# Optimization experiments

Measured on AMD Instinct MI355X. Metric: run time of the kernel, lower is better.

The kernel has to match this reference:

```python
import jax, jax.numpy as jnp
import numpy as np

SIZE = 1024
LATENT_DIM = 256
BETA_C = 0.25
LEGACY = True


def setup_inputs() -> dict:
    key = jax.random.key(0)
    k1, k2 = jax.random.split(key)
    z = jax.random.normal(k1, (8, LATENT_DIM, 16, 16, 16), dtype=jnp.float32)
    # nn.Embedding weight initialized uniform(-1/size, 1/size)
    embedding = jax.random.uniform(
        k2, (SIZE, LATENT_DIM), minval=-1.0 / SIZE, maxval=1.0 / SIZE, dtype=jnp.float32
    )
    return {"z": z, "embedding": embedding}


def reference(z, embedding):
    sg = jax.lax.stop_gradient
    B, C, D, H, W = z.shape
    # [B, D, H, W, C]
    zp = jnp.transpose(z, (0, 2, 3, 4, 1))
    zf = zp.reshape(-1, C)  # [N, C]
    # pairwise squared distances [N, K]
    d = (
        jnp.sum(zf * zf, axis=1, keepdims=True)
        + jnp.sum(embedding * embedding, axis=1)
        - 2.0 * (zf @ embedding.T)
    )
    idx = jnp.argmin(d, axis=1)  # [N]
    # direct gather == one-hot @ embedding
    z_q = embedding[idx].reshape(zp.shape)
    if LEGACY:
        loss = jnp.mean((sg(z_q) - zp) ** 2) + BETA_C * jnp.mean((z_q - sg(zp)) ** 2)
    else:
        loss = BETA_C * jnp.mean((sg(z_q) - zp) ** 2) + jnp.mean((z_q - sg(zp)) ** 2)
    # perplexity: e_mean = mean of one-hot encodings == normalized counts
    counts = jnp.zeros((SIZE,), dtype=z.dtype).at[idx].add(1.0)
    e_mean = counts / zf.shape[0]
    perplexity = jnp.exp(-jnp.sum(e_mean * jnp.log(e_mean + 1e-10)))
    # straight-through estimator
    z_q = zp + sg(z_q - zp)
    z_q = jnp.transpose(z_q, (0, 4, 1, 2, 3))  # back to [B, C, D, H, W]
    return z_q, loss, perplexity, idx
```

## Files before the change

kernel.cpp:

```cpp
#include <hip/hip_runtime.h>
#include <cstddef>
#include <cstdint>

#define CDIM 256
#define SPAT 4096
#define KCODE 1024

#define LOSS_OFF 8388608
#define PERP_OFF 8388609
#define IDX_OFF  8388610

typedef __bf16 bf16x8 __attribute__((ext_vector_type(8)));
typedef float floatx16 __attribute__((ext_vector_type(16)));
typedef unsigned short ushort8 __attribute__((ext_vector_type(8)));

__device__ __forceinline__ unsigned short f2bf_rne(float f) {
    union { float f; uint32_t u; } c; c.f = f;
    uint32_t u = c.u;
    return (unsigned short)((u + 0x7fffu + ((u >> 16) & 1u)) >> 16);
}
__device__ __forceinline__ float bf2f(unsigned short h) {
    union { float f; uint32_t u; } c; c.u = ((uint32_t)h) << 16;
    return c.f;
}

__device__ __forceinline__ void dma16(const void* g, void* l) {
    __builtin_amdgcn_global_load_lds(
        (const __attribute__((address_space(1))) void*)g,
        (__attribute__((address_space(3))) void*)l, 16, 0, 0);
}

__global__ __launch_bounds__(256) void vq_prep(const float* __restrict__ emb,
                                               unsigned short* __restrict__ ehsw,
                                               unsigned short* __restrict__ elsw,
                                               float* __restrict__ enorm,
                                               float* __restrict__ counts,
                                               float* __restrict__ losssum,
                                               unsigned long long* __restrict__ pbm) {
    int tid = threadIdx.x;
    if (blockIdx.x == 0) {
        for (int i = tid; i < KCODE; i += 256) counts[i] = 0.0f;
        if (tid == 0) losssum[0] = 0.0f;
    }
    if (tid < 128) pbm[blockIdx.x * 128 + tid] = 0xFFFFFFFFFFFFFFFFull;

    int w = tid >> 6, lane = tid & 63;
    int k = blockIdx.x * 4 + w;
    const float* row = emb + (size_t)k * CDIM;
    float s = 0.0f;
#pragma unroll
    for (int i = 0; i < 4; ++i) {
        float v = row[lane + 64 * i];
        s = fmaf(v, v, s);
    }
#pragma unroll
    for (int m = 32; m > 0; m >>= 1) s += __shfl_xor(s, m, 64);
    if (lane == 0) enorm[k] = s;

    float4 v4 = *(const float4*)(row + lane * 4);
    unsigned short h0 = f2bf_rne(v4.x), h1 = f2bf_rne(v4.y),
                   h2 = f2bf_rne(v4.z), h3 = f2bf_rne(v4.w);
    ushort4 hv = make_ushort4(h0, h1, h2, h3);
    ushort4 lv = make_ushort4(f2bf_rne(v4.x - bf2f(h0)), f2bf_rne(v4.y - bf2f(h1)),
                              f2bf_rne(v4.z - bf2f(h2)), f2bf_rne(v4.w - bf2f(h3)));
    int kb = lane >> 1, cj = (lane & 1) * 4;
    int st = k >> 5, ks = k & 31;
    int phys = kb ^ (ks & 7);
    size_t dst = (size_t)st * 8192 + ks * 256 + phys * 8 + cj;
    *(ushort4*)(ehsw + dst) = hv;
    *(ushort4*)(elsw + dst) = lv;
}

__global__ __launch_bounds__(256, 2) void vq_dist(const float* __restrict__ z,
                                                  const unsigned short* __restrict__ ehsw,
                                                  const unsigned short* __restrict__ elsw,
                                                  const float* __restrict__ enorm,
                                                  unsigned long long* __restrict__ pbm) {
    __shared__ __align__(16) unsigned char lds[65536 + 2048 + 512];
    float* zhalf = (float*)lds;
    float* ens_s = (float*)(lds + 65536);
    float* zzs   = (float*)(lds + 67584);

    const int tid = threadIdx.x;
    const int w = tid >> 6;
    const int lane = tid & 63;
    const int m_ = lane & 31;
    const int g = lane >> 5;
    const int bid = blockIdx.x;
    const int pos = bid >> 1;
    const int kh = bid & 1;
    const int ch = w & 1;
    const int hlf = w >> 1;
    const int n0 = pos * 128;
    const int b = n0 >> 12;
    const int sp0 = n0 & 4095;
    const float* zb = z + (size_t)b * CDIM * SPAT + sp0;
    const int stg0 = (bid >> 4) & 15;

    ushort8 zh[16], zl[16];

    for (int h = 0; h < 2; ++h) {
        for (int i = tid; i < CDIM * 16; i += 256) {
            int c = i >> 4, seg = i & 15;
            *(float4*)&zhalf[c * 64 + seg * 4] =
                *(const float4*)(zb + (size_t)c * SPAT + h * 64 + seg * 4);
        }
        __syncthreads();
        if (hlf == h) {
#pragma unroll
            for (int kc = 0; kc < 16; ++kc) {
#pragma unroll
                for (int j = 0; j < 8; ++j) {
                    float v = zhalf[(kc * 16 + g * 8 + j) * 64 + ch * 32 + m_];
                    unsigned short hb = f2bf_rne(v);
                    unsigned short lb = f2bf_rne(v - bf2f(hb));
                    zh[kc][j] = hb; zl[kc][j] = lb;
                }
            }
        } else if (w == (h == 0 ? 2 : 0)) {
            float s = 0.0f;
            for (int c = 0; c < CDIM; ++c) {
                float v = zhalf[c * 64 + lane];
                s = fmaf(v, v, s);
            }
            zzs[h * 64 + lane] = s;
        } else if (h == 0 && w == 3) {
            for (int i = lane; i < 512; i += 64) ens_s[i] = enorm[kh * 512 + i];
        }
        __syncthreads();
    }

    const float zzv = zzs[w * 32 + m_];

    float bs = 3.4e38f;
    int bi_ = 0;

    const int bufid = w >> 1;
    const int hf = w & 1;
    const char* gsrc = (const char*)(bufid ? elsw : ehsw);
    const int gs0 = kh * 16;

    {
        const char* gp = gsrc + ((size_t)(gs0 + stg0) << 14) + (hf << 13) + (lane << 4);
        char* lp = (char*)lds + ((size_t)bufid << 14) + (hf << 13);
#pragma unroll
        for (int j = 0; j < 8; ++j) dma16(gp + j * 1024, lp + j * 1024);
    }

    for (int s = 0; s < 16; ++s) {
        __syncthreads();
        if (s < 15) {
            const int se_n = (s + 1 + stg0) & 15;
            const char* gp = gsrc + ((size_t)(gs0 + se_n) << 14) + (hf << 13) + (lane << 4);
            char* lp = (char*)lds + (((size_t)(s + 1) & 1) << 15) +
                       ((size_t)bufid << 14) + (hf << 13);
#pragma unroll
            for (int j = 0; j < 8; ++j) dma16(gp + j * 1024, lp + j * 1024);
            __builtin_amdgcn_sched_barrier(0);
        }
        const char* EHb = (const char*)lds + (((size_t)s & 1) << 15);
        const char* ELb = EHb + 16384;

        floatx16 a = {0.0f, 0.0f, 0.0f, 0.0f, 0.0f, 0.0f, 0.0f, 0.0f,
                      0.0f, 0.0f, 0.0f, 0.0f, 0.0f, 0.0f, 0.0f, 0.0f};
#pragma unroll
        for (int kc = 0; kc < 16; ++kc) {
            int kb0 = kc * 2 + g;
            int off = m_ * 512 + ((kb0 ^ (m_ & 7)) << 4);
            bf16x8 aeh = *(const bf16x8*)(EHb + off);
            bf16x8 ael = *(const bf16x8*)(ELb + off);
            bf16x8 bh = __builtin_bit_cast(bf16x8, zh[kc]);
            bf16x8 bl = __builtin_bit_cast(bf16x8, zl[kc]);
            a = __builtin_amdgcn_mfma_f32_32x32x16_bf16(aeh, bh, a, 0, 0, 0);
            a = __builtin_amdgcn_mfma_f32_32x32x16_bf16(ael, bh, a, 0, 0, 0);
            a = __builtin_amdgcn_mfma_f32_32x32x16_bf16(aeh, bl, a, 0, 0, 0);
        }

        const int se = (s + stg0) & 15;
#pragma unroll
        for (int reg = 0; reg < 16; ++reg) {
            int mm = (reg & 3) + 8 * (reg >> 2) + 4 * g;
            int il = se * 32 + mm;
            float en = ens_s[il];
            float d = (zzv + en) - 2.0f * a[reg];
            int code = kh * 512 + il;
            if (d < bs || (d == bs && code < bi_)) { bs = d; bi_ = code; }
        }
    }

    {
        float s2 = __shfl_xor(bs, 32, 64);
        int i2 = __shfl_xor(bi_, 32, 64);
        if (s2 < bs || (s2 == bs && i2 < bi_)) { bs = s2; bi_ = i2; }
    }
    if (lane < 32) {
        unsigned long long key =
            ((unsigned long long)__float_as_uint(bs) << 32) | (unsigned int)bi_;
        atomicMin(&pbm[n0 + w * 32 + m_], key);
    }
}

__global__ __launch_bounds__(256) void vq_gather(const float* __restrict__ z,
                                                 const float* __restrict__ emb,
                                                 const unsigned long long* __restrict__ pbm,
                                                 float* __restrict__ counts,
                                                 float* __restrict__ losssum,
                                                 float* __restrict__ out) {
    __shared__ __align__(16) unsigned char lds[128 * 1040 + 512];
    int* bidxs = (int*)(lds + 133120);

    const int tid = threadIdx.x;
    const int w = tid >> 6;
    const int lane = tid & 63;
    const int n0 = blockIdx.x * 128;
    const int b = n0 >> 12;
    const int sp0 = n0 & 4095;
    const float* zb = z + (size_t)b * CDIM * SPAT + sp0;

    if (tid < 128) {
        int ki = (int)(unsigned int)(pbm[n0 + tid] & 0xFFFFFFFFull);
        bidxs[tid] = ki;
        out[IDX_OFF + n0 + tid] = (float)ki;
        atomicAdd(&counts[ki], 1.0f);
    }
    __syncthreads();

#pragma unroll
    for (int r = 0; r < 32; ++r) {
        int row = w * 32 + r;
        int k = bidxs[row];
        int slot = (row & 3) * 32 + (row >> 2);
        dma16((const char*)emb + ((size_t)k << 10) + (lane << 4),
              (char*)lds + (size_t)slot * 1040);
    }
    __syncthreads();

    float ls = 0.0f;
    float* outz = out + (size_t)b * CDIM * SPAT + sp0;
    const int col4 = tid & 31;
    const int c_0 = tid >> 5;
    const float* e0 = (const float*)((const char*)lds + (size_t)(0 * 32 + col4) * 1040);
    const float* e1 = (const float*)((const char*)lds + (size_t)(1 * 32 + col4) * 1040);
    const float* e2 = (const float*)((const char*)lds + (size_t)(2 * 32 + col4) * 1040);
    const float* e3 = (const float*)((const char*)lds + (size_t)(3 * 32 + col4) * 1040);
    for (int c = c_0; c < CDIM; c += 8) {
        float4 zp = *(const float4*)(zb + (size_t)c * SPAT + col4 * 4);
        float d0 = e0[c] - zp.x, d1 = e1[c] - zp.y,
              d2 = e2[c] - zp.z, d3 = e3[c] - zp.w;
        float4 o;
        o.x = zp.x + d0; o.y = zp.y + d1; o.z = zp.z + d2; o.w = zp.w + d3;
        ls = fmaf(d0, d0, ls); ls = fmaf(d1, d1, ls);
        ls = fmaf(d2, d2, ls); ls = fmaf(d3, d3, ls);
        *(float4*)(outz + (size_t)c * SPAT + col4 * 4) = o;
    }
#pragma unroll
    for (int m = 32; m > 0; m >>= 1) ls += __shfl_xor(ls, m, 64);
    if (lane == 0) atomicAdd(losssum, ls);
}

__global__ __launch_bounds__(256) void vq_finalize(const float* __restrict__ counts,
                                                   const float* __restrict__ losssum,
                                                   float* __restrict__ out) {
    __shared__ float red[256];
    int tid = threadIdx.x;
    float s = 0.0f;
    for (int k = tid; k < KCODE; k += 256) {
        float em = counts[k] * (1.0f / 32768.0f);
        s += em * logf(em + 1e-10f);
    }
    red[tid] = s;
    __syncthreads();
    for (int off = 128; off > 0; off >>= 1) {
        if (tid < off) red[tid] += red[tid + off];
        __syncthreads();
    }
    if (tid == 0) {
        float m = losssum[0] * (1.0f / 8388608.0f);
        out[LOSS_OFF] = m + 0.25f * m;
        out[PERP_OFF] = expf(-red[0]);
    }
}

extern "C" void kernel_launch(void* const* d_in, const int* in_sizes, int n_in,
                              void* d_out, int out_size, void* d_ws, size_t ws_size,
                              hipStream_t stream) {
    const float* z = (const float*)d_in[0];
    const float* emb = (const float*)d_in[1];
    float* out = (float*)d_out;
    unsigned long long* pbm = (unsigned long long*)d_ws;
    unsigned short* ehsw = (unsigned short*)(pbm + 32768);
    unsigned short* elsw = ehsw + (size_t)KCODE * CDIM;
    float* enorm = (float*)(elsw + (size_t)KCODE * CDIM);
    float* counts = enorm + KCODE;
    float* losssum = counts + KCODE;

    vq_prep<<<256, 256, 0, stream>>>(emb, ehsw, elsw, enorm, counts, losssum, pbm);
    vq_dist<<<512, 256, 0, stream>>>(z, ehsw, elsw, enorm, pbm);
    vq_gather<<<256, 256, 0, stream>>>(z, emb, pbm, counts, losssum, out);
    vq_finalize<<<1, 256, 0, stream>>>(counts, losssum, out);
}
```

Before: 179.8 us.

## Fuse gather epilogue into distance kernel via last-block-arrives flag

```diff
diff --git a/kernel.cpp b/kernel.cpp
--- a/kernel.cpp
+++ b/kernel.cpp
@@ -36,12 +36,14 @@
                                                float* __restrict__ enorm,
                                                float* __restrict__ counts,
                                                float* __restrict__ losssum,
-                                               unsigned long long* __restrict__ pbm) {
+                                               unsigned long long* __restrict__ pbm,
+                                               unsigned int* __restrict__ flags) {
     int tid = threadIdx.x;
     if (blockIdx.x == 0) {
         for (int i = tid; i < KCODE; i += 256) counts[i] = 0.0f;
         if (tid == 0) losssum[0] = 0.0f;
     }
+    if (blockIdx.x == 1) flags[tid] = 0u;
     if (tid < 128) pbm[blockIdx.x * 128 + tid] = 0xFFFFFFFFFFFFFFFFull;
 
     int w = tid >> 6, lane = tid & 63;
@@ -72,14 +74,20 @@
 }
 
 __global__ __launch_bounds__(256, 2) void vq_dist(const float* __restrict__ z,
+                                                  const float* __restrict__ emb,
                                                   const unsigned short* __restrict__ ehsw,
                                                   const unsigned short* __restrict__ elsw,
                                                   const float* __restrict__ enorm,
-                                                  unsigned long long* __restrict__ pbm) {
+                                                  unsigned long long* __restrict__ pbm,
+                                                  unsigned int* __restrict__ flags,
+                                                  float* __restrict__ counts,
+                                                  float* __restrict__ losssum,
+                                                  float* __restrict__ out) {
     __shared__ __align__(16) unsigned char lds[65536 + 2048 + 512];
     float* zhalf = (float*)lds;
     float* ens_s = (float*)(lds + 65536);
     float* zzs   = (float*)(lds + 67584);
+    __shared__ int last_s;
 
     const int tid = threadIdx.x;
     const int w = tid >> 6;
@@ -198,60 +206,56 @@
             ((unsigned long long)__float_as_uint(bs) << 32) | (unsigned int)bi_;
         atomicMin(&pbm[n0 + w * 32 + m_], key);
     }
-}
-
-__global__ __launch_bounds__(256) void vq_gather(const float* __restrict__ z,
-                                                 const float* __restrict__ emb,
-                                                 const unsigned long long* __restrict__ pbm,
-                                                 float* __restrict__ counts,
-                                                 float* __restrict__ losssum,
-                                                 float* __restrict__ out) {
-    __shared__ __align__(16) unsigned char lds[128 * 1040 + 512];
-    int* bidxs = (int*)(lds + 133120);
-
-    const int tid = threadIdx.x;
-    const int w = tid >> 6;
-    const int lane = tid & 63;
-    const int n0 = blockIdx.x * 128;
-    const int b = n0 >> 12;
-    const int sp0 = n0 & 4095;
-    const float* zb = z + (size_t)b * CDIM * SPAT + sp0;
-
+    __threadfence();
+    __syncthreads();
+    if (tid == 0) last_s = (atomicAdd(&flags[pos], 1u) == 1u);
+    __syncthreads();
+    if (!last_s) return;
+    __threadfence();
+
+    int* bidxs = (int*)(lds + 67584);
     if (tid < 128) {
-        int ki = (int)(unsigned int)(pbm[n0 + tid] & 0xFFFFFFFFull);
+        unsigned long long key = __hip_atomic_load(
+            &pbm[n0 + tid], __ATOMIC_RELAXED, __HIP_MEMORY_SCOPE_AGENT);
+        int ki = (int)(unsigned int)(key & 0xFFFFFFFFull);
         bidxs[tid] = ki;
         out[IDX_OFF + n0 + tid] = (float)ki;
         atomicAdd(&counts[ki], 1.0f);
     }
     __syncthreads();
 
-#pragma unroll
-    for (int r = 0; r < 32; ++r) {
-        int row = w * 32 + r;
-        int k = bidxs[row];
-        int slot = (row & 3) * 32 + (row >> 2);
-        dma16((const char*)emb + ((size_t)k << 10) + (lane << 4),
-              (char*)lds + (size_t)slot * 1040);
-    }
-    __syncthreads();
-
     float ls = 0.0f;
     float* outz = out + (size_t)b * CDIM * SPAT + sp0;
     const int col4 = tid & 31;
-    const int c_0 = tid >> 5;
-    const float* e0 = (const float*)((const char*)lds + (size_t)(0 * 32 + col4) * 1040);
-    const float* e1 = (const float*)((const char*)lds + (size_t)(1 * 32 + col4) * 1040);
-    const float* e2 = (const float*)((const char*)lds + (size_t)(2 * 32 + col4) * 1040);
-    const float* e3 = (const float*)((const char*)lds + (size_t)(3 * 32 + col4) * 1040);
-    for (int c = c_0; c < CDIM; c += 8) {
-        float4 zp = *(const float4*)(zb + (size_t)c * SPAT + col4 * 4);
-        float d0 = e0[c] - zp.x, d1 = e1[c] - zp.y,
-              d2 = e2[c] - zp.z, d3 = e3[c] - zp.w;
-        float4 o;
-        o.x = zp.x + d0; o.y = zp.y + d1; o.z = zp.z + d2; o.w = zp.w + d3;
-        ls = fmaf(d0, d0, ls); ls = fmaf(d1, d1, ls);
-        ls = fmaf(d2, d2, ls); ls = fmaf(d3, d3, ls);
-        *(float4*)(outz + (size_t)c * SPAT + col4 * 4) = o;
+    const int c_0t = tid >> 5;
+    const int col4h = col4 & 15;
+    for (int round = 0; round < 2; ++round) {
+#pragma unroll
+        for (int r = 0; r < 16; ++r) {
+            int row_local = w * 16 + r;
+            int k = bidxs[round * 64 + row_local];
+            int slot = (row_local & 3) * 16 + (row_local >> 2);
+            dma16((const char*)emb + ((size_t)k << 10) + (lane << 4),
+                  (char*)lds + (size_t)slot * 1040);
+        }
+        __syncthreads();
+        if ((col4 >> 4) == round) {
+            const float* e0 = (const float*)((const char*)lds + (size_t)(0 * 16 + col4h) * 1040);
+            const float* e1 = (const float*)((const char*)lds + (size_t)(1 * 16 + col4h) * 1040);
+            const float* e2 = (const float*)((const char*)lds + (size_t)(2 * 16 + col4h) * 1040);
+            const float* e3 = (const float*)((const char*)lds + (size_t)(3 * 16 + col4h) * 1040);
+            for (int c = c_0t; c < CDIM; c += 8) {
+                float4 zp = *(const float4*)(zb + (size_t)c * SPAT + col4 * 4);
+                float d0 = e0[c] - zp.x, d1 = e1[c] - zp.y,
+                      d2 = e2[c] - zp.z, d3 = e3[c] - zp.w;
+                float4 o;
+                o.x = zp.x + d0; o.y = zp.y + d1; o.z = zp.z + d2; o.w = zp.w + d3;
+                ls = fmaf(d0, d0, ls); ls = fmaf(d1, d1, ls);
+                ls = fmaf(d2, d2, ls); ls = fmaf(d3, d3, ls);
+                *(float4*)(outz + (size_t)c * SPAT + col4 * 4) = o;
+            }
+        }
+        __syncthreads();
     }
 #pragma unroll
     for (int m = 32; m > 0; m >>= 1) ls += __shfl_xor(ls, m, 64);
@@ -293,9 +297,10 @@
     float* enorm = (float*)(elsw + (size_t)KCODE * CDIM);
     float* counts = enorm + KCODE;
     float* losssum = counts + KCODE;
-
-    vq_prep<<<256, 256, 0, stream>>>(emb, ehsw, elsw, enorm, counts, losssum, pbm);
-    vq_dist<<<512, 256, 0, stream>>>(z, ehsw, elsw, enorm, pbm);
-    vq_gather<<<256, 256, 0, stream>>>(z, emb, pbm, counts, losssum, out);
+    unsigned int* flags = (unsigned int*)(losssum + 1);
+
+    vq_prep<<<256, 256, 0, stream>>>(emb, ehsw, elsw, enorm, counts, losssum, pbm, flags);
+    vq_dist<<<512, 256, 0, stream>>>(z, emb, ehsw, elsw, enorm, pbm, flags,
+                                     counts, losssum, out);
     vq_finalize<<<1, 256, 0, stream>>>(counts, losssum, out);
 }
```

Result: slower. 228.0 us (+26.8%).
